# Kernel tuning notes

Hardware: AMD Instinct MI355X
Metric: run time of the kernel (lower is better)

Reference implementation:

```python
import jax, jax.numpy as jnp
import numpy as np

N_HEADS = 4
HEAD_DIM = 32
N_GROUPS = 32
EPS = 1e-5


def setup_inputs() -> dict:
    key = jax.random.key(0)
    ks = jax.random.split(key, 4)
    B, C, H, W = 2, 128, 64, 64
    x = jax.random.normal(ks[0], (B, C, H, W), dtype=jnp.float32)
    t = jax.random.normal(ks[1], (B,), dtype=jnp.float32)
    norm_w = jnp.ones((C,), dtype=jnp.float32)
    norm_b = jnp.zeros((C,), dtype=jnp.float32)
    proj_w = jax.random.normal(ks[2], (3 * N_HEADS * HEAD_DIM, C), dtype=jnp.float32) * 0.02
    proj_b = jnp.zeros((3 * N_HEADS * HEAD_DIM,), dtype=jnp.float32)
    out_w = jax.random.normal(ks[3], (C, N_HEADS * HEAD_DIM), dtype=jnp.float32) * 0.02
    out_b = jnp.zeros((C,), dtype=jnp.float32)
    return {"x": x, "t": t, "norm_w": norm_w, "norm_b": norm_b,
            "proj_w": proj_w, "proj_b": proj_b, "out_w": out_w, "out_b": out_b}


def reference(x, t, norm_w, norm_b, proj_w, proj_b, out_w, out_b):
    B, C = x.shape[0], x.shape[1]
    Hh, d = N_HEADS, HEAD_DIM
    scale = d ** -0.5
    # GroupNorm over (channels-per-group, spatial)
    xg = x.reshape(B, N_GROUPS, -1)
    mean = jnp.mean(xg, axis=-1, keepdims=True)
    var = jnp.var(xg, axis=-1, keepdims=True)
    xn = ((xg - mean) * jax.lax.rsqrt(var + EPS)).reshape(x.shape)
    xn = xn * norm_w[None, :, None, None] + norm_b[None, :, None, None]
    # tokens: [B, N, C]
    h = xn.reshape(B, C, -1).transpose(0, 2, 1)
    x_tok = x.reshape(B, C, -1).transpose(0, 2, 1)  # residual (pre-norm)
    N = h.shape[1]
    qkv = (h @ proj_w.T + proj_b).reshape(B, N, Hh, 3 * d)
    q, k, v = jnp.split(qkv, 3, axis=-1)  # each [B, N, H, d]
    attn = jnp.einsum('bihd,bjhd->bijh', q, k) * scale  # [B, N, N, H]
    attn = jax.nn.softmax(attn, axis=2)
    out = jnp.einsum('bijh,bjhd->bihd', attn, v).reshape(B, N, Hh * d)
    out = out @ out_w.T + out_b
    return out + x_tok  # [B, N, C]
```

## Files before the change

### kernel.cpp

```cpp
#include <hip/hip_runtime.h>
#include <hip/hip_bf16.h>

typedef __bf16 bf16x8 __attribute__((ext_vector_type(8)));
typedef __bf16 bf16x4 __attribute__((ext_vector_type(4)));
typedef float f32x4 __attribute__((ext_vector_type(4)));

#define QSCALE (0.17677669529663689f * 1.44269504088896340736f)

__device__ __forceinline__ f32x4 mfma_16x16x32(bf16x8 a, bf16x8 b, f32x4 c) {
  return __builtin_amdgcn_mfma_f32_16x16x32_bf16(a, b, c, 0, 0, 0);
}

__global__ __launch_bounds__(256) void prep_kernel(
    const float* __restrict__ x, float* __restrict__ stats,
    const float* __restrict__ pw, const float* __restrict__ ow,
    __bf16* __restrict__ Wp, __bf16* __restrict__ Wq) {
  if (blockIdx.x < 64) {
    int bg = blockIdx.x;
    const f32x4* base = (const f32x4*)(x + (size_t)bg * 16384);
    float s = 0.f, ss = 0.f;
    for (int i = threadIdx.x; i < 4096; i += 256) {
      f32x4 v = base[i];
      s += v[0] + v[1] + v[2] + v[3];
      ss += v[0]*v[0] + v[1]*v[1] + v[2]*v[2] + v[3]*v[3];
    }
    #pragma unroll
    for (int off = 32; off; off >>= 1) {
      s += __shfl_down(s, off);
      ss += __shfl_down(ss, off);
    }
    __shared__ float rs[4], rss[4];
    int wid = threadIdx.x >> 6;
    if ((threadIdx.x & 63) == 0) { rs[wid] = s; rss[wid] = ss; }
    __syncthreads();
    if (threadIdx.x == 0) {
      float S = rs[0] + rs[1] + rs[2] + rs[3];
      float SS = rss[0] + rss[1] + rss[2] + rss[3];
      float mean = S * (1.f / 16384.f);
      float var = SS * (1.f / 16384.f) - mean * mean;
      stats[bg * 2] = mean;
      stats[bg * 2 + 1] = rsqrtf(var + 1e-5f);
    }
    return;
  }
  int idx = (blockIdx.x - 64) * 256 + threadIdx.x;
  const float* src;
  __bf16* dst;
  if (idx < 6144) {
    int lane = idx & 63, ks = (idx >> 6) & 3;
    int rest = idx >> 8;
    int ot = rest % 6, hh = rest / 6;
    src = pw + (size_t)(hh * 96 + ot * 16 + (lane & 15)) * 128 + ks * 32 +
          8 * (lane >> 4);
    dst = Wp + (size_t)idx * 8;
  } else {
    int j = idx - 6144;
    int lane = j & 63, ks = (j >> 6) & 3;
    int rest = j >> 8;
    int ot = rest & 1, wv = rest >> 1;
    src = ow + (size_t)(wv * 32 + ot * 16 + (lane & 15)) * 128 + ks * 32 +
          8 * (lane >> 4);
    dst = Wq + (size_t)j * 8;
  }
  f32x4 a = *(const f32x4*)src;
  f32x4 b2 = *(const f32x4*)(src + 4);
  bf16x8 w;
  #pragma unroll
  for (int i = 0; i < 4; ++i) { w[i] = (__bf16)a[i]; w[4 + i] = (__bf16)b2[i]; }
  *(bf16x8*)dst = w;
}

__global__ __launch_bounds__(256) void qkv_kernel(
    const float* __restrict__ x, const float* __restrict__ stats,
    const float* __restrict__ nw, const float* __restrict__ nb,
    const __bf16* __restrict__ Wp, const float* __restrict__ pb,
    __bf16* __restrict__ Qb, __bf16* __restrict__ Kp, __bf16* __restrict__ Vb) {
  __shared__ __bf16 ht[16 * 128];
  int chunk = blockIdx.x & 255;
  int b = blockIdx.x >> 8;
  int tid = threadIdx.x;
  int n0 = chunk * 16;
  {
    int c = tid >> 1, hf = tid & 1;
    const float* xs = x + ((size_t)b * 128 + c) * 4096 + n0 + hf * 8;
    f32x4 x0 = *(const f32x4*)xs;
    f32x4 x1 = *(const f32x4*)(xs + 4);
    float mean = stats[(b * 32 + (c >> 2)) * 2];
    float rstd = stats[(b * 32 + (c >> 2)) * 2 + 1];
    float wsc = nw[c], bsc = nb[c];
    #pragma unroll
    for (int j = 0; j < 8; ++j) {
      float v = (j < 4) ? x0[j] : x1[j - 4];
      float hv = (v - mean) * rstd * wsc + bsc;
      int tok = hf * 8 + j;
      int byte = (tok * 256 + c * 2) ^ ((tok & 7) << 4);
      *(__bf16*)((char*)ht + byte) = (__bf16)hv;
    }
  }
  int wave = tid >> 6, lane = tid & 63;
  int g = lane >> 4, r = lane & 15;
  int hh = wave;
  bf16x8 wf[6][4];
  const bf16x8* wpp = (const bf16x8*)Wp;
  #pragma unroll
  for (int ot = 0; ot < 6; ++ot)
    #pragma unroll
    for (int ks = 0; ks < 4; ++ks)
      wf[ot][ks] = wpp[((hh * 6 + ot) * 4 + ks) * 64 + lane];
  __syncthreads();
  bf16x8 bfr[4];
  #pragma unroll
  for (int ks = 0; ks < 4; ++ks) {
    int byte = (r * 256 + (ks * 32 + 8 * g) * 2) ^ ((r & 7) << 4);
    bfr[ks] = *(const bf16x8*)((char*)ht + byte);
  }
  f32x4 acc[6];
  #pragma unroll
  for (int ot = 0; ot < 6; ++ot) acc[ot] = (f32x4){0.f, 0.f, 0.f, 0.f};
  #pragma unroll
  for (int ks = 0; ks < 4; ++ks)
    #pragma unroll
    for (int ot = 0; ot < 6; ++ot)
      acc[ot] = mfma_16x16x32(wf[ot][ks], bfr[ks], acc[ot]);
  int bh = b * 4 + hh;
  int n = n0 + r;
  #pragma unroll
  for (int ot = 0; ot < 6; ++ot) {
    int o_lo = ot * 16 + 4 * g;
    f32x4 bias = *(const f32x4*)(pb + hh * 96 + o_lo);
    f32x4 v = acc[ot];
    if (ot < 2) {
      bf16x4 qv;
      #pragma unroll
      for (int i = 0; i < 4; ++i) qv[i] = (__bf16)((v[i] + bias[i]) * QSCALE);
      *(bf16x4*)(Qb + ((size_t)bh * 4096 + n) * 32 + o_lo) = qv;
    } else if (ot < 4) {
      bf16x4 kv;
      #pragma unroll
      for (int i = 0; i < 4; ++i) kv[i] = (__bf16)(v[i] + bias[i]);
      size_t koff = ((size_t)(bh * 128 + (n >> 5))) * 1024 +
                    (size_t)((n >> 4) & 1) * 512 +
                    ((n & 15) + 16 * ((ot - 2) * 2 + (g >> 1))) * 8 +
                    (g & 1) * 4;
      *(bf16x4*)(Kp + koff) = kv;
    } else {
      #pragma unroll
      for (int i = 0; i < 4; ++i) {
        int d = o_lo - 64 + i;
        int jr = n & 31, jb2 = n >> 5;
        int reg = ((jr >> 4) << 2) | (jr & 3);
        int gg = (jr >> 2) & 3;
        int half = d >> 4;
        int lane2 = gg * 16 + (d & 15);
        Vb[(((size_t)bh * 128 + jb2) * 2 + half) * 512 + lane2 * 8 + reg] =
            (__bf16)(v[i] + bias[i]);
      }
    }
  }
}

__global__ __launch_bounds__(256) void attn_kernel(
    const __bf16* __restrict__ Qb, const __bf16* __restrict__ Kp,
    const __bf16* __restrict__ Vb, __bf16* __restrict__ Op,
    float* __restrict__ Lp) {
  __shared__ __bf16 kls[3][1024];
  __shared__ __bf16 vls[3][1024];
  int bh = blockIdx.x & 7;
  int rest = blockIdx.x >> 3;
  int ks = rest & 3;
  int qt = rest >> 2;
  int wave = threadIdx.x >> 6;
  int lane = threadIdx.x & 63;
  int g = lane >> 4, r = lane & 15;
  int qi = qt * 128 + wave * 32 + r;
  bf16x8 qf0 = *(const bf16x8*)(Qb + ((size_t)bh * 4096 + qi) * 32 + 8 * g);
  bf16x8 qf1 = *(const bf16x8*)(Qb + ((size_t)bh * 4096 + qi + 16) * 32 + 8 * g);
  const __bf16* ktile = Kp + (size_t)bh * 131072;
  const __bf16* vtile = Vb + (size_t)bh * 131072;
  bf16x8 ones;
  #pragma unroll
  for (int i = 0; i < 8; ++i) ones[i] = (__bf16)1.0f;
  f32x4 acc00 = {0.f,0.f,0.f,0.f}, acc01 = {0.f,0.f,0.f,0.f};
  f32x4 acc10 = {0.f,0.f,0.f,0.f}, acc11 = {0.f,0.f,0.f,0.f};
  f32x4 accd0 = {0.f,0.f,0.f,0.f}, accd1 = {0.f,0.f,0.f,0.f};
  int jb0 = ks * 32;
  auto stage = [&](int buf, int jb) {
    const __bf16* src;
    __bf16* dst;
    if (wave < 2) {
      src = ktile + jb * 1024 + wave * 512 + lane * 8;
      dst = &kls[buf][wave * 512];
    } else {
      src = vtile + jb * 1024 + (wave - 2) * 512 + lane * 8;
      dst = &vls[buf][(wave - 2) * 512];
    }
    __builtin_amdgcn_global_load_lds(
        (const __attribute__((address_space(1))) uint32_t*)src,
        (__attribute__((address_space(3))) uint32_t*)dst, 16, 0, 0);
  };
  stage(0, jb0);
  stage(1, jb0 + 1);
  for (int t = 0; t < 32; ++t) {
    asm volatile("s_waitcnt vmcnt(1)" ::: "memory");
    __builtin_amdgcn_sched_barrier(0);
    __builtin_amdgcn_s_barrier();
    int buf = t % 3;
    bf16x8 kc0 = *(const bf16x8*)&kls[buf][lane * 8];
    bf16x8 kc1 = *(const bf16x8*)&kls[buf][512 + lane * 8];
    bf16x8 vc0 = *(const bf16x8*)&vls[buf][lane * 8];
    bf16x8 vc1 = *(const bf16x8*)&vls[buf][512 + lane * 8];
    f32x4 z = {0.f, 0.f, 0.f, 0.f};
    f32x4 s00 = mfma_16x16x32(kc0, qf0, z);
    f32x4 s01 = mfma_16x16x32(kc1, qf0, z);
    f32x4 s10 = mfma_16x16x32(kc0, qf1, z);
    f32x4 s11 = mfma_16x16x32(kc1, qf1, z);
    float p0[8], p1[8];
    #pragma unroll
    for (int i = 0; i < 4; ++i) {
      p0[i]     = __builtin_amdgcn_exp2f(s00[i]);
      p0[4 + i] = __builtin_amdgcn_exp2f(s01[i]);
      p1[i]     = __builtin_amdgcn_exp2f(s10[i]);
      p1[4 + i] = __builtin_amdgcn_exp2f(s11[i]);
    }
    bf16x8 pf0, pf1;
    #pragma unroll
    for (int i = 0; i < 8; ++i) { pf0[i] = (__bf16)p0[i]; pf1[i] = (__bf16)p1[i]; }
    acc00 = mfma_16x16x32(vc0, pf0, acc00);
    acc01 = mfma_16x16x32(vc1, pf0, acc01);
    acc10 = mfma_16x16x32(vc0, pf1, acc10);
    acc11 = mfma_16x16x32(vc1, pf1, acc11);
    accd0 = mfma_16x16x32(ones, pf0, accd0);
    accd1 = mfma_16x16x32(ones, pf1, accd1);
    int nt = t + 2;
    stage(nt % 3, jb0 + (nt & 31));
  }
  size_t base = (size_t)(ks * 8 + bh) * 4096 + qi;
  bf16x4 o00, o01, o10, o11;
  #pragma unroll
  for (int i = 0; i < 4; ++i) {
    o00[i] = (__bf16)acc00[i]; o01[i] = (__bf16)acc01[i];
    o10[i] = (__bf16)acc10[i]; o11[i] = (__bf16)acc11[i];
  }
  *(bf16x4*)(Op + base * 32 + 4 * g) = o00;
  *(bf16x4*)(Op + base * 32 + 16 + 4 * g) = o01;
  *(bf16x4*)(Op + (base + 16) * 32 + 4 * g) = o10;
  *(bf16x4*)(Op + (base + 16) * 32 + 16 + 4 * g) = o11;
  if (g == 0) { Lp[base] = accd0[0]; Lp[base + 16] = accd1[0]; }
}

__global__ __launch_bounds__(256) void proj_out_kernel(
    const __bf16* __restrict__ Op, const float* __restrict__ Lp,
    const __bf16* __restrict__ Wq, const float* __restrict__ ob,
    const float* __restrict__ x, float* __restrict__ out) {
  __shared__ __bf16 ol[2048];
  __shared__ float rl[16][4];
  __shared__ float xl[128][20];
  int b = blockIdx.x >> 8;
  int n0 = (blockIdx.x & 255) * 16;
  int tid = threadIdx.x;
  if (tid < 64) {
    int t = tid >> 2, hh = tid & 3;
    size_t qidx = (size_t)(b * 4 + hh) * 4096 + n0 + t;
    float l = Lp[qidx] + Lp[qidx + 8 * 4096] + Lp[qidx + 16 * 4096] +
              Lp[qidx + 24 * 4096];
    rl[t][hh] = 1.f / l;
  }
  {
    int c = tid >> 1, hf = tid & 1;
    const float* xs = x + ((size_t)b * 128 + c) * 4096 + n0 + hf * 8;
    f32x4 x0 = *(const f32x4*)xs;
    f32x4 x1 = *(const f32x4*)(xs + 4);
    *(f32x4*)&xl[c][hf * 8] = x0;
    *(f32x4*)&xl[c][hf * 8 + 4] = x1;
  }
  __syncthreads();
  {
    int t = tid >> 4, p8 = (tid & 15) * 8;
    int hh = p8 >> 5;
    size_t base = ((size_t)(b * 4 + hh) * 4096 + n0 + t) * 32 + (p8 & 31);
    float s[8] = {0.f, 0.f, 0.f, 0.f, 0.f, 0.f, 0.f, 0.f};
    #pragma unroll
    for (int ks = 0; ks < 4; ++ks) {
      bf16x8 v = *(const bf16x8*)(Op + base + (size_t)ks * 1048576);
      #pragma unroll
      for (int j = 0; j < 8; ++j) s[j] += (float)v[j];
    }
    float sc = rl[t][hh];
    bf16x8 ob8;
    #pragma unroll
    for (int j = 0; j < 8; ++j) ob8[j] = (__bf16)(s[j] * sc);
    int byte = (t * 256 + p8 * 2) ^ ((t & 7) << 4);
    *(bf16x8*)((char*)ol + byte) = ob8;
  }
  __syncthreads();
  int wave = tid >> 6, lane = tid & 63;
  int g = lane >> 4, r = lane & 15;
  bf16x8 bfr[4];
  #pragma unroll
  for (int ks = 0; ks < 4; ++ks) {
    int byte = (r * 256 + ks * 64 + g * 16) ^ ((r & 7) << 4);
    bfr[ks] = *(const bf16x8*)((char*)ol + byte);
  }
  const bf16x8* wqp = (const bf16x8*)Wq;
  f32x4 acc[2];
  #pragma unroll
  for (int ot = 0; ot < 2; ++ot) {
    acc[ot] = (f32x4){0.f, 0.f, 0.f, 0.f};
    #pragma unroll
    for (int ks = 0; ks < 4; ++ks)
      acc[ot] = mfma_16x16x32(wqp[((wave * 2 + ot) * 4 + ks) * 64 + lane],
                              bfr[ks], acc[ot]);
  }
  int n = n0 + r;
  #pragma unroll
  for (int ot = 0; ot < 2; ++ot) {
    int c0 = wave * 32 + ot * 16 + 4 * g;
    f32x4 bias = *(const f32x4*)(ob + c0);
    f32x4 o = acc[ot];
    #pragma unroll
    for (int i = 0; i < 4; ++i) o[i] += bias[i] + xl[c0 + i][r];
    *(f32x4*)(out + ((size_t)b * 4096 + n) * 128 + c0) = o;
  }
}

extern "C" void kernel_launch(void* const* d_in, const int* in_sizes, int n_in,
                              void* d_out, int out_size, void* d_ws, size_t ws_size,
                              hipStream_t stream) {
  const float* x  = (const float*)d_in[0];
  const float* nw = (const float*)d_in[2];
  const float* nb = (const float*)d_in[3];
  const float* pw = (const float*)d_in[4];
  const float* pb = (const float*)d_in[5];
  const float* ow = (const float*)d_in[6];
  const float* ob = (const float*)d_in[7];
  float* out = (float*)d_out;

  char* ws = (char*)d_ws;
  float* stats = (float*)ws;
  __bf16* Qb = (__bf16*)(ws + 1024);
  __bf16* Kp = (__bf16*)(ws + 1024 + 2097152);
  __bf16* Vb = (__bf16*)(ws + 1024 + 4194304);
  __bf16* Op = (__bf16*)(ws + 1024 + 6291456);
  float*  Lp = (float*)(ws + 1024 + 14680064);
  __bf16* Wp = (__bf16*)(ws + 1024 + 15204352);
  __bf16* Wq = (__bf16*)(ws + 1024 + 15302656);

  prep_kernel<<<96, 256, 0, stream>>>(x, stats, pw, ow, Wp, Wq);
  qkv_kernel<<<512, 256, 0, stream>>>(x, stats, nw, nb, Wp, pb, Qb, Kp, Vb);
  attn_kernel<<<1024, 256, 0, stream>>>(Qb, Kp, Vb, Op, Lp);
  proj_out_kernel<<<512, 256, 0, stream>>>(Op, Lp, Wq, ob, x, out);
}
```

Baseline: 119.7 us.

## Fuse four kernels into one cooperative persistent kernel with grid syncs

Replaces the prep, QKV, attention and output-projection launches with a single cooperative kernel of 512 blocks that separates the phases with grid.sync. The attention phase is re-tiled so each wave handles 64 queries instead of 32, which halves the block count and gives each loaded K/V tile more reuse. The goal is to remove launch gaps and inter-kernel drain between the stages. The costs are grid-wide barrier overhead, higher register pressure from the larger attention tile under launch_bounds(256,2), and less latency hiding in attention from having fewer blocks.

```diff
diff --git a/kernel.cpp b/kernel.cpp
--- a/kernel.cpp
+++ b/kernel.cpp
@@ -1,5 +1,8 @@
 #include <hip/hip_runtime.h>
 #include <hip/hip_bf16.h>
+#include <hip/hip_cooperative_groups.h>
+
+namespace cg = cooperative_groups;
 
 typedef __bf16 bf16x8 __attribute__((ext_vector_type(8)));
 typedef __bf16 bf16x4 __attribute__((ext_vector_type(4)));
@@ -11,15 +14,26 @@
   return __builtin_amdgcn_mfma_f32_16x16x32_bf16(a, b, c, 0, 0, 0);
 }
 
-__global__ __launch_bounds__(256) void prep_kernel(
-    const float* __restrict__ x, float* __restrict__ stats,
-    const float* __restrict__ pw, const float* __restrict__ ow,
+__global__ __launch_bounds__(256, 2) void mega_kernel(
+    const float* __restrict__ x, const float* __restrict__ nw,
+    const float* __restrict__ nb, const float* __restrict__ pw,
+    const float* __restrict__ pb, const float* __restrict__ ow,
+    const float* __restrict__ ob, float* __restrict__ out,
+    float* __restrict__ stats, __bf16* __restrict__ Qb,
+    __bf16* __restrict__ Kp, __bf16* __restrict__ Vb,
+    __bf16* __restrict__ Op, float* __restrict__ Lp,
     __bf16* __restrict__ Wp, __bf16* __restrict__ Wq) {
-  if (blockIdx.x < 64) {
-    int bg = blockIdx.x;
+  cg::grid_group grid = cg::this_grid();
+  __shared__ __align__(16) char smraw[14592];
+  int blk = blockIdx.x, tid = threadIdx.x;
+  int wave = tid >> 6, lane = tid & 63;
+  int g = lane >> 4, r = lane & 15;
+
+  if (blk < 64) {
+    int bg = blk;
     const f32x4* base = (const f32x4*)(x + (size_t)bg * 16384);
     float s = 0.f, ss = 0.f;
-    for (int i = threadIdx.x; i < 4096; i += 256) {
+    for (int i = tid; i < 4096; i += 256) {
       f32x4 v = base[i];
       s += v[0] + v[1] + v[2] + v[3];
       ss += v[0]*v[0] + v[1]*v[1] + v[2]*v[2] + v[3]*v[3];
@@ -29,11 +43,11 @@
       s += __shfl_down(s, off);
       ss += __shfl_down(ss, off);
     }
-    __shared__ float rs[4], rss[4];
-    int wid = threadIdx.x >> 6;
-    if ((threadIdx.x & 63) == 0) { rs[wid] = s; rss[wid] = ss; }
+    float* rs = (float*)smraw;
+    float* rss = rs + 4;
+    if ((tid & 63) == 0) { rs[wave] = s; rss[wave] = ss; }
     __syncthreads();
-    if (threadIdx.x == 0) {
+    if (tid == 0) {
       float S = rs[0] + rs[1] + rs[2] + rs[3];
       float SS = rss[0] + rss[1] + rss[2] + rss[3];
       float mean = S * (1.f / 16384.f);
@@ -41,285 +55,274 @@
       stats[bg * 2] = mean;
       stats[bg * 2 + 1] = rsqrtf(var + 1e-5f);
     }
-    return;
+  } else if (blk < 96) {
+    int idx = (blk - 64) * 256 + tid;
+    const float* src;
+    __bf16* dst;
+    if (idx < 6144) {
+      int ln = idx & 63, ks = (idx >> 6) & 3;
+      int rest = idx >> 8;
+      int ot = rest % 6, hh = rest / 6;
+      src = pw + (size_t)(hh * 96 + ot * 16 + (ln & 15)) * 128 + ks * 32 +
+            8 * (ln >> 4);
+      dst = Wp + (size_t)idx * 8;
+    } else {
+      int j = idx - 6144;
+      int ln = j & 63, ks = (j >> 6) & 3;
+      int rest = j >> 8;
+      int ot = rest & 1, wv = rest >> 1;
+      src = ow + (size_t)(wv * 32 + ot * 16 + (ln & 15)) * 128 + ks * 32 +
+            8 * (ln >> 4);
+      dst = Wq + (size_t)j * 8;
+    }
+    f32x4 a = *(const f32x4*)src;
+    f32x4 b2 = *(const f32x4*)(src + 4);
+    bf16x8 w;
+    #pragma unroll
+    for (int i = 0; i < 4; ++i) { w[i] = (__bf16)a[i]; w[4 + i] = (__bf16)b2[i]; }
+    *(bf16x8*)dst = w;
   }
-  int idx = (blockIdx.x - 64) * 256 + threadIdx.x;
-  const float* src;
-  __bf16* dst;
-  if (idx < 6144) {
-    int lane = idx & 63, ks = (idx >> 6) & 3;
-    int rest = idx >> 8;
-    int ot = rest % 6, hh = rest / 6;
-    src = pw + (size_t)(hh * 96 + ot * 16 + (lane & 15)) * 128 + ks * 32 +
-          8 * (lane >> 4);
-    dst = Wp + (size_t)idx * 8;
-  } else {
-    int j = idx - 6144;
-    int lane = j & 63, ks = (j >> 6) & 3;
-    int rest = j >> 8;
-    int ot = rest & 1, wv = rest >> 1;
-    src = ow + (size_t)(wv * 32 + ot * 16 + (lane & 15)) * 128 + ks * 32 +
-          8 * (lane >> 4);
-    dst = Wq + (size_t)j * 8;
+  __threadfence();
+  grid.sync();
+
+  {
+    __bf16* ht = (__bf16*)smraw;
+    int chunk = blk & 255;
+    int b = blk >> 8;
+    int n0 = chunk * 16;
+    {
+      int c = tid >> 1, hf = tid & 1;
+      const float* xs = x + ((size_t)b * 128 + c) * 4096 + n0 + hf * 8;
+      f32x4 x0 = *(const f32x4*)xs;
+      f32x4 x1 = *(const f32x4*)(xs + 4);
+      float mean = stats[(b * 32 + (c >> 2)) * 2];
+      float rstd = stats[(b * 32 + (c >> 2)) * 2 + 1];
+      float wsc = nw[c], bsc = nb[c];
+      #pragma unroll
+      for (int j = 0; j < 8; ++j) {
+        float v = (j < 4) ? x0[j] : x1[j - 4];
+        float hv = (v - mean) * rstd * wsc + bsc;
+        int tok = hf * 8 + j;
+        int byte = (tok * 256 + c * 2) ^ ((tok & 7) << 4);
+        *(__bf16*)((char*)ht + byte) = (__bf16)hv;
+      }
+    }
+    int hh = wave;
+    bf16x8 wf[6][4];
+    const bf16x8* wpp = (const bf16x8*)Wp;
+    #pragma unroll
+    for (int ot = 0; ot < 6; ++ot)
+      #pragma unroll
+      for (int ks = 0; ks < 4; ++ks)
+        wf[ot][ks] = wpp[((hh * 6 + ot) * 4 + ks) * 64 + lane];
+    __syncthreads();
+    bf16x8 bfr[4];
+    #pragma unroll
+    for (int ks = 0; ks < 4; ++ks) {
+      int byte = (r * 256 + (ks * 32 + 8 * g) * 2) ^ ((r & 7) << 4);
+      bfr[ks] = *(const bf16x8*)((char*)ht + byte);
+    }
+    f32x4 acc[6];
+    #pragma unroll
+    for (int ot = 0; ot < 6; ++ot) acc[ot] = (f32x4){0.f, 0.f, 0.f, 0.f};
+    #pragma unroll
+    for (int ks = 0; ks < 4; ++ks)
+      #pragma unroll
+      for (int ot = 0; ot < 6; ++ot)
+        acc[ot] = mfma_16x16x32(wf[ot][ks], bfr[ks], acc[ot]);
+    int bh = b * 4 + hh;
+    int n = n0 + r;
+    #pragma unroll
+    for (int ot = 0; ot < 6; ++ot) {
+      int o_lo = ot * 16 + 4 * g;
+      f32x4 bias = *(const f32x4*)(pb + hh * 96 + o_lo);
+      f32x4 v = acc[ot];
+      if (ot < 2) {
+        bf16x4 qv;
+        #pragma unroll
+        for (int i = 0; i < 4; ++i) qv[i] = (__bf16)((v[i] + bias[i]) * QSCALE);
+        *(bf16x4*)(Qb + ((size_t)bh * 4096 + n) * 32 + o_lo) = qv;
+      } else if (ot < 4) {
+        bf16x4 kv;
+        #pragma unroll
+        for (int i = 0; i < 4; ++i) kv[i] = (__bf16)(v[i] + bias[i]);
+        size_t koff = ((size_t)(bh * 128 + (n >> 5))) * 1024 +
+                      (size_t)((n >> 4) & 1) * 512 +
+                      ((n & 15) + 16 * ((ot - 2) * 2 + (g >> 1))) * 8 +
+                      (g & 1) * 4;
+        *(bf16x4*)(Kp + koff) = kv;
+      } else {
+        #pragma unroll
+        for (int i = 0; i < 4; ++i) {
+          int d = o_lo - 64 + i;
+          int jr = n & 31, jb2 = n >> 5;
+          int reg = ((jr >> 4) << 2) | (jr & 3);
+          int gg = (jr >> 2) & 3;
+          int half = d >> 4;
+          int lane2 = gg * 16 + (d & 15);
+          Vb[(((size_t)bh * 128 + jb2) * 2 + half) * 512 + lane2 * 8 + reg] =
+              (__bf16)(v[i] + bias[i]);
+        }
+      }
+    }
   }
-  f32x4 a = *(const f32x4*)src;
-  f32x4 b2 = *(const f32x4*)(src + 4);
-  bf16x8 w;
-  #pragma unroll
-  for (int i = 0; i < 4; ++i) { w[i] = (__bf16)a[i]; w[4 + i] = (__bf16)b2[i]; }
-  *(bf16x8*)dst = w;
-}
-
-__global__ __launch_bounds__(256) void qkv_kernel(
-    const float* __restrict__ x, const float* __restrict__ stats,
-    const float* __restrict__ nw, const float* __restrict__ nb,
-    const __bf16* __restrict__ Wp, const float* __restrict__ pb,
-    __bf16* __restrict__ Qb, __bf16* __restrict__ Kp, __bf16* __restrict__ Vb) {
-  __shared__ __bf16 ht[16 * 128];
-  int chunk = blockIdx.x & 255;
-  int b = blockIdx.x >> 8;
-  int tid = threadIdx.x;
-  int n0 = chunk * 16;
+  __threadfence();
+  grid.sync();
+
   {
-    int c = tid >> 1, hf = tid & 1;
-    const float* xs = x + ((size_t)b * 128 + c) * 4096 + n0 + hf * 8;
-    f32x4 x0 = *(const f32x4*)xs;
-    f32x4 x1 = *(const f32x4*)(xs + 4);
-    float mean = stats[(b * 32 + (c >> 2)) * 2];
-    float rstd = stats[(b * 32 + (c >> 2)) * 2 + 1];
-    float wsc = nw[c], bsc = nb[c];
-    #pragma unroll
-    for (int j = 0; j < 8; ++j) {
-      float v = (j < 4) ? x0[j] : x1[j - 4];
-      float hv = (v - mean) * rstd * wsc + bsc;
-      int tok = hf * 8 + j;
-      int byte = (tok * 256 + c * 2) ^ ((tok & 7) << 4);
-      *(__bf16*)((char*)ht + byte) = (__bf16)hv;
+    int bh = blk & 7;
+    int ks = (blk >> 3) & 3;
+    int qt = blk >> 5;
+    int qi = qt * 256 + wave * 64 + r;
+    const __bf16* qbase = Qb + ((size_t)bh * 4096 + qi) * 32 + 8 * g;
+    bf16x8 qf[4];
+    #pragma unroll
+    for (int j = 0; j < 4; ++j) qf[j] = *(const bf16x8*)(qbase + j * 512);
+    const __bf16* ktile = Kp + (size_t)bh * 131072;
+    const __bf16* vtile = Vb + (size_t)bh * 131072;
+    __bf16* kls = (__bf16*)smraw;
+    __bf16* vls = (__bf16*)(smraw + 6144);
+    bf16x8 ones;
+    #pragma unroll
+    for (int i = 0; i < 8; ++i) ones[i] = (__bf16)1.0f;
+    f32x4 acc[4][2], accd[4];
+    #pragma unroll
+    for (int j = 0; j < 4; ++j) {
+      acc[j][0] = (f32x4){0.f, 0.f, 0.f, 0.f};
+      acc[j][1] = (f32x4){0.f, 0.f, 0.f, 0.f};
+      accd[j] = (f32x4){0.f, 0.f, 0.f, 0.f};
+    }
+    int jb0 = ks * 32;
+    auto stage = [&](int buf, int jb) {
+      const __bf16* src;
+      __bf16* dst;
+      if (wave < 2) {
+        src = ktile + jb * 1024 + wave * 512 + lane * 8;
+        dst = kls + buf * 1024 + wave * 512;
+      } else {
+        src = vtile + jb * 1024 + (wave - 2) * 512 + lane * 8;
+        dst = vls + buf * 1024 + (wave - 2) * 512;
+      }
+      __builtin_amdgcn_global_load_lds(
+          (const __attribute__((address_space(1))) uint32_t*)src,
+          (__attribute__((address_space(3))) uint32_t*)dst, 16, 0, 0);
+    };
+    stage(0, jb0);
+    stage(1, jb0 + 1);
+    for (int t = 0; t < 32; ++t) {
+      asm volatile("s_waitcnt vmcnt(1)" ::: "memory");
+      __builtin_amdgcn_sched_barrier(0);
+      __builtin_amdgcn_s_barrier();
+      int buf = t % 3;
+      bf16x8 kc0 = *(const bf16x8*)(kls + buf * 1024 + lane * 8);
+      bf16x8 kc1 = *(const bf16x8*)(kls + buf * 1024 + 512 + lane * 8);
+      bf16x8 vc0 = *(const bf16x8*)(vls + buf * 1024 + lane * 8);
+      bf16x8 vc1 = *(const bf16x8*)(vls + buf * 1024 + 512 + lane * 8);
+      #pragma unroll
+      for (int j = 0; j < 4; ++j) {
+        f32x4 z = {0.f, 0.f, 0.f, 0.f};
+        f32x4 s0 = mfma_16x16x32(kc0, qf[j], z);
+        f32x4 s1 = mfma_16x16x32(kc1, qf[j], z);
+        float p[8];
+        #pragma unroll
+        for (int i = 0; i < 4; ++i) {
+          p[i]     = __builtin_amdgcn_exp2f(s0[i]);
+          p[4 + i] = __builtin_amdgcn_exp2f(s1[i]);
+        }
+        bf16x8 pf;
+        #pragma unroll
+        for (int i = 0; i < 8; ++i) pf[i] = (__bf16)p[i];
+        acc[j][0] = mfma_16x16x32(vc0, pf, acc[j][0]);
+        acc[j][1] = mfma_16x16x32(vc1, pf, acc[j][1]);
+        accd[j]  = mfma_16x16x32(ones, pf, accd[j]);
+      }
+      int nt = t + 2;
+      stage(nt % 3, jb0 + (nt & 31));
+    }
+    #pragma unroll
+    for (int j = 0; j < 4; ++j) {
+      size_t base = (size_t)(ks * 8 + bh) * 4096 + qi + 16 * j;
+      bf16x4 o0, o1;
+      #pragma unroll
+      for (int i = 0; i < 4; ++i) {
+        o0[i] = (__bf16)acc[j][0][i];
+        o1[i] = (__bf16)acc[j][1][i];
+      }
+      *(bf16x4*)(Op + base * 32 + 4 * g) = o0;
+      *(bf16x4*)(Op + base * 32 + 16 + 4 * g) = o1;
+      if (g == 0) Lp[base] = accd[j][0];
     }
   }
-  int wave = tid >> 6, lane = tid & 63;
-  int g = lane >> 4, r = lane & 15;
-  int hh = wave;
-  bf16x8 wf[6][4];
-  const bf16x8* wpp = (const bf16x8*)Wp;
-  #pragma unroll
-  for (int ot = 0; ot < 6; ++ot)
-    #pragma unroll
-    for (int ks = 0; ks < 4; ++ks)
-      wf[ot][ks] = wpp[((hh * 6 + ot) * 4 + ks) * 64 + lane];
-  __syncthreads();
-  bf16x8 bfr[4];
-  #pragma unroll
-  for (int ks = 0; ks < 4; ++ks) {
-    int byte = (r * 256 + (ks * 32 + 8 * g) * 2) ^ ((r & 7) << 4);
-    bfr[ks] = *(const bf16x8*)((char*)ht + byte);
-  }
-  f32x4 acc[6];
-  #pragma unroll
-  for (int ot = 0; ot < 6; ++ot) acc[ot] = (f32x4){0.f, 0.f, 0.f, 0.f};
-  #pragma unroll
-  for (int ks = 0; ks < 4; ++ks)
-    #pragma unroll
-    for (int ot = 0; ot < 6; ++ot)
-      acc[ot] = mfma_16x16x32(wf[ot][ks], bfr[ks], acc[ot]);
-  int bh = b * 4 + hh;
-  int n = n0 + r;
-  #pragma unroll
-  for (int ot = 0; ot < 6; ++ot) {
-    int o_lo = ot * 16 + 4 * g;
-    f32x4 bias = *(const f32x4*)(pb + hh * 96 + o_lo);
-    f32x4 v = acc[ot];
-    if (ot < 2) {
-      bf16x4 qv;
-      #pragma unroll
-      for (int i = 0; i < 4; ++i) qv[i] = (__bf16)((v[i] + bias[i]) * QSCALE);
-      *(bf16x4*)(Qb + ((size_t)bh * 4096 + n) * 32 + o_lo) = qv;
-    } else if (ot < 4) {
-      bf16x4 kv;
-      #pragma unroll
-      for (int i = 0; i < 4; ++i) kv[i] = (__bf16)(v[i] + bias[i]);
-      size_t koff = ((size_t)(bh * 128 + (n >> 5))) * 1024 +
-                    (size_t)((n >> 4) & 1) * 512 +
-                    ((n & 15) + 16 * ((ot - 2) * 2 + (g >> 1))) * 8 +
-                    (g & 1) * 4;
-      *(bf16x4*)(Kp + koff) = kv;
-    } else {
-      #pragma unroll
-      for (int i = 0; i < 4; ++i) {
-        int d = o_lo - 64 + i;
-        int jr = n & 31, jb2 = n >> 5;
-        int reg = ((jr >> 4) << 2) | (jr & 3);
-        int gg = (jr >> 2) & 3;
-        int half = d >> 4;
-        int lane2 = gg * 16 + (d & 15);
-        Vb[(((size_t)bh * 128 + jb2) * 2 + half) * 512 + lane2 * 8 + reg] =
-            (__bf16)(v[i] + bias[i]);
-      }
-    }
-  }
-}
-
-__global__ __launch_bounds__(256) void attn_kernel(
-    const __bf16* __restrict__ Qb, const __bf16* __restrict__ Kp,
-    const __bf16* __restrict__ Vb, __bf16* __restrict__ Op,
-    float* __restrict__ Lp) {
-  __shared__ __bf16 kls[3][1024];
-  __shared__ __bf16 vls[3][1024];
-  int bh = blockIdx.x & 7;
-  int rest = blockIdx.x >> 3;
-  int ks = rest & 3;
-  int qt = rest >> 2;
-  int wave = threadIdx.x >> 6;
-  int lane = threadIdx.x & 63;
-  int g = lane >> 4, r = lane & 15;
-  int qi = qt * 128 + wave * 32 + r;
-  bf16x8 qf0 = *(const bf16x8*)(Qb + ((size_t)bh * 4096 + qi) * 32 + 8 * g);
-  bf16x8 qf1 = *(const bf16x8*)(Qb + ((size_t)bh * 4096 + qi + 16) * 32 + 8 * g);
-  const __bf16* ktile = Kp + (size_t)bh * 131072;
-  const __bf16* vtile = Vb + (size_t)bh * 131072;
-  bf16x8 ones;
-  #pragma unroll
-  for (int i = 0; i < 8; ++i) ones[i] = (__bf16)1.0f;
-  f32x4 acc00 = {0.f,0.f,0.f,0.f}, acc01 = {0.f,0.f,0.f,0.f};
-  f32x4 acc10 = {0.f,0.f,0.f,0.f}, acc11 = {0.f,0.f,0.f,0.f};
-  f32x4 accd0 = {0.f,0.f,0.f,0.f}, accd1 = {0.f,0.f,0.f,0.f};
-  int jb0 = ks * 32;
-  auto stage = [&](int buf, int jb) {
-    const __bf16* src;
-    __bf16* dst;
-    if (wave < 2) {
-      src = ktile + jb * 1024 + wave * 512 + lane * 8;
-      dst = &kls[buf][wave * 512];
-    } else {
-      src = vtile + jb * 1024 + (wave - 2) * 512 + lane * 8;
-      dst = &vls[buf][(wave - 2) * 512];
-    }
-    __builtin_amdgcn_global_load_lds(
-        (const __attribute__((address_space(1))) uint32_t*)src,
-        (__attribute__((address_space(3))) uint32_t*)dst, 16, 0, 0);
-  };
-  stage(0, jb0);
-  stage(1, jb0 + 1);
-  for (int t = 0; t < 32; ++t) {
-    asm volatile("s_waitcnt vmcnt(1)" ::: "memory");
-    __builtin_amdgcn_sched_barrier(0);
-    __builtin_amdgcn_s_barrier();
-    int buf = t % 3;
-    bf16x8 kc0 = *(const bf16x8*)&kls[buf][lane * 8];
-    bf16x8 kc1 = *(const bf16x8*)&kls[buf][512 + lane * 8];
-    bf16x8 vc0 = *(const bf16x8*)&vls[buf][lane * 8];
-    bf16x8 vc1 = *(const bf16x8*)&vls[buf][512 + lane * 8];
-    f32x4 z = {0.f, 0.f, 0.f, 0.f};
-    f32x4 s00 = mfma_16x16x32(kc0, qf0, z);
-    f32x4 s01 = mfma_16x16x32(kc1, qf0, z);
-    f32x4 s10 = mfma_16x16x32(kc0, qf1, z);
-    f32x4 s11 = mfma_16x16x32(kc1, qf1, z);
-    float p0[8], p1[8];
-    #pragma unroll
-    for (int i = 0; i < 4; ++i) {
-      p0[i]     = __builtin_amdgcn_exp2f(s00[i]);
-      p0[4 + i] = __builtin_amdgcn_exp2f(s01[i]);
-      p1[i]     = __builtin_amdgcn_exp2f(s10[i]);
-      p1[4 + i] = __builtin_amdgcn_exp2f(s11[i]);
-    }
-    bf16x8 pf0, pf1;
-    #pragma unroll
-    for (int i = 0; i < 8; ++i) { pf0[i] = (__bf16)p0[i]; pf1[i] = (__bf16)p1[i]; }
-    acc00 = mfma_16x16x32(vc0, pf0, acc00);
-    acc01 = mfma_16x16x32(vc1, pf0, acc01);
-    acc10 = mfma_16x16x32(vc0, pf1, acc10);
-    acc11 = mfma_16x16x32(vc1, pf1, acc11);
-    accd0 = mfma_16x16x32(ones, pf0, accd0);
-    accd1 = mfma_16x16x32(ones, pf1, accd1);
-    int nt = t + 2;
-    stage(nt % 3, jb0 + (nt & 31));
-  }
-  size_t base = (size_t)(ks * 8 + bh) * 4096 + qi;
-  bf16x4 o00, o01, o10, o11;
-  #pragma unroll
-  for (int i = 0; i < 4; ++i) {
-    o00[i] = (__bf16)acc00[i]; o01[i] = (__bf16)acc01[i];
-    o10[i] = (__bf16)acc10[i]; o11[i] = (__bf16)acc11[i];
-  }
-  *(bf16x4*)(Op + base * 32 + 4 * g) = o00;
-  *(bf16x4*)(Op + base * 32 + 16 + 4 * g) = o01;
-  *(bf16x4*)(Op + (base + 16) * 32 + 4 * g) = o10;
-  *(bf16x4*)(Op + (base + 16) * 32 + 16 + 4 * g) = o11;
-  if (g == 0) { Lp[base] = accd0[0]; Lp[base + 16] = accd1[0]; }
-}
-
-__global__ __launch_bounds__(256) void proj_out_kernel(
-    const __bf16* __restrict__ Op, const float* __restrict__ Lp,
-    const __bf16* __restrict__ Wq, const float* __restrict__ ob,
-    const float* __restrict__ x, float* __restrict__ out) {
-  __shared__ __bf16 ol[2048];
-  __shared__ float rl[16][4];
-  __shared__ float xl[128][20];
-  int b = blockIdx.x >> 8;
-  int n0 = (blockIdx.x & 255) * 16;
-  int tid = threadIdx.x;
-  if (tid < 64) {
-    int t = tid >> 2, hh = tid & 3;
-    size_t qidx = (size_t)(b * 4 + hh) * 4096 + n0 + t;
-    float l = Lp[qidx] + Lp[qidx + 8 * 4096] + Lp[qidx + 16 * 4096] +
-              Lp[qidx + 24 * 4096];
-    rl[t][hh] = 1.f / l;
-  }
+  __threadfence();
+  grid.sync();
+
   {
-    int c = tid >> 1, hf = tid & 1;
-    const float* xs = x + ((size_t)b * 128 + c) * 4096 + n0 + hf * 8;
-    f32x4 x0 = *(const f32x4*)xs;
-    f32x4 x1 = *(const f32x4*)(xs + 4);
-    *(f32x4*)&xl[c][hf * 8] = x0;
-    *(f32x4*)&xl[c][hf * 8 + 4] = x1;
-  }
-  __syncthreads();
-  {
-    int t = tid >> 4, p8 = (tid & 15) * 8;
-    int hh = p8 >> 5;
-    size_t base = ((size_t)(b * 4 + hh) * 4096 + n0 + t) * 32 + (p8 & 31);
-    float s[8] = {0.f, 0.f, 0.f, 0.f, 0.f, 0.f, 0.f, 0.f};
+    __bf16* ol = (__bf16*)smraw;
+    float (*rl)[4] = (float(*)[4])(smraw + 4096);
+    float (*xl)[20] = (float(*)[20])(smraw + 4352);
+    int b = blk >> 8;
+    int n0 = (blk & 255) * 16;
+    if (tid < 64) {
+      int t = tid >> 2, hh = tid & 3;
+      size_t qidx = (size_t)(b * 4 + hh) * 4096 + n0 + t;
+      float l = Lp[qidx] + Lp[qidx + 8 * 4096] + Lp[qidx + 16 * 4096] +
+                Lp[qidx + 24 * 4096];
+      rl[t][hh] = 1.f / l;
+    }
+    {
+      int c = tid >> 1, hf = tid & 1;
+      const float* xs = x + ((size_t)b * 128 + c) * 4096 + n0 + hf * 8;
+      f32x4 x0 = *(const f32x4*)xs;
+      f32x4 x1 = *(const f32x4*)(xs + 4);
+      *(f32x4*)&xl[c][hf * 8] = x0;
+      *(f32x4*)&xl[c][hf * 8 + 4] = x1;
+    }
+    __syncthreads();
+    {
+      int t = tid >> 4, p8 = (tid & 15) * 8;
+      int hh = p8 >> 5;
+      size_t base = ((size_t)(b * 4 + hh) * 4096 + n0 + t) * 32 + (p8 & 31);
+      float s[8] = {0.f, 0.f, 0.f, 0.f, 0.f, 0.f, 0.f, 0.f};
+      #pragma unroll
+      for (int ks = 0; ks < 4; ++ks) {
+        bf16x8 v = *(const bf16x8*)(Op + base + (size_t)ks * 1048576);
+        #pragma unroll
+        for (int j = 0; j < 8; ++j) s[j] += (float)v[j];
+      }
+      float sc = rl[t][hh];
+      bf16x8 ob8;
+      #pragma unroll
+      for (int j = 0; j < 8; ++j) ob8[j] = (__bf16)(s[j] * sc);
+      int byte = (t * 256 + p8 * 2) ^ ((t & 7) << 4);
+      *(bf16x8*)((char*)ol + byte) = ob8;
+    }
+    __syncthreads();
+    bf16x8 bfr[4];
     #pragma unroll
     for (int ks = 0; ks < 4; ++ks) {
-      bf16x8 v = *(const bf16x8*)(Op + base + (size_t)ks * 1048576);
-      #pragma unroll
-      for (int j = 0; j < 8; ++j) s[j] += (float)v[j];
-    }
-    float sc = rl[t][hh];
-    bf16x8 ob8;
-    #pragma unroll
-    for (int j = 0; j < 8; ++j) ob8[j] = (__bf16)(s[j] * sc);
-    int byte = (t * 256 + p8 * 2) ^ ((t & 7) << 4);
-    *(bf16x8*)((char*)ol + byte) = ob8;
-  }
-  __syncthreads();
-  int wave = tid >> 6, lane = tid & 63;
-  int g = lane >> 4, r = lane & 15;
-  bf16x8 bfr[4];
-  #pragma unroll
-  for (int ks = 0; ks < 4; ++ks) {
-    int byte = (r * 256 + ks * 64 + g * 16) ^ ((r & 7) << 4);
-    bfr[ks] = *(const bf16x8*)((char*)ol + byte);
-  }
-  const bf16x8* wqp = (const bf16x8*)Wq;
-  f32x4 acc[2];
-  #pragma unroll
-  for (int ot = 0; ot < 2; ++ot) {
-    acc[ot] = (f32x4){0.f, 0.f, 0.f, 0.f};
-    #pragma unroll
-    for (int ks = 0; ks < 4; ++ks)
-      acc[ot] = mfma_16x16x32(wqp[((wave * 2 + ot) * 4 + ks) * 64 + lane],
-                              bfr[ks], acc[ot]);
-  }
-  int n = n0 + r;
-  #pragma unroll
-  for (int ot = 0; ot < 2; ++ot) {
-    int c0 = wave * 32 + ot * 16 + 4 * g;
-    f32x4 bias = *(const f32x4*)(ob + c0);
-    f32x4 o = acc[ot];
-    #pragma unroll
-    for (int i = 0; i < 4; ++i) o[i] += bias[i] + xl[c0 + i][r];
-    *(f32x4*)(out + ((size_t)b * 4096 + n) * 128 + c0) = o;
+      int byte = (r * 256 + ks * 64 + g * 16) ^ ((r & 7) << 4);
+      bfr[ks] = *(const bf16x8*)((char*)ol + byte);
+    }
+    const bf16x8* wqp = (const bf16x8*)Wq;
+    f32x4 acc[2];
+    #pragma unroll
+    for (int ot = 0; ot < 2; ++ot) {
+      acc[ot] = (f32x4){0.f, 0.f, 0.f, 0.f};
+      #pragma unroll
+      for (int ks = 0; ks < 4; ++ks)
+        acc[ot] = mfma_16x16x32(wqp[((wave * 2 + ot) * 4 + ks) * 64 + lane],
+                                bfr[ks], acc[ot]);
+    }
+    int n = n0 + r;
+    #pragma unroll
+    for (int ot = 0; ot < 2; ++ot) {
+      int c0 = wave * 32 + ot * 16 + 4 * g;
+      f32x4 bias = *(const f32x4*)(ob + c0);
+      f32x4 o = acc[ot];
+      #pragma unroll
+      for (int i = 0; i < 4; ++i) o[i] += bias[i] + xl[c0 + i][r];
+      *(f32x4*)(out + ((size_t)b * 4096 + n) * 128 + c0) = o;
+    }
   }
 }
 
@@ -345,8 +348,8 @@
   __bf16* Wp = (__bf16*)(ws + 1024 + 15204352);
   __bf16* Wq = (__bf16*)(ws + 1024 + 15302656);
 
-  prep_kernel<<<96, 256, 0, stream>>>(x, stats, pw, ow, Wp, Wq);
-  qkv_kernel<<<512, 256, 0, stream>>>(x, stats, nw, nb, Wp, pb, Qb, Kp, Vb);
-  attn_kernel<<<1024, 256, 0, stream>>>(Qb, Kp, Vb, Op, Lp);
-  proj_out_kernel<<<512, 256, 0, stream>>>(Op, Lp, Wq, ob, x, out);
+  void* args[] = {&x, &nw, &nb, &pw, &pb, &ow, &ob, &out,
+                  &stats, &Qb, &Kp, &Vb, &Op, &Lp, &Wp, &Wq};
+  hipLaunchCooperativeKernel((void*)mega_kernel, dim3(512), dim3(256),
+                             args, 0, stream);
 }
```

Result: slower. 464.9 us (+288.3%).
